# Kernel tuning notes

Measured on AMD Instinct MI355X. Metric: run time of the kernel, lower is better.

The kernel has to match this reference:

```python
import jax, jax.numpy as jnp
import numpy as np

B = 8
INPUT_SIZE = 32        # fc output dim == res row length
RESAMPLING = 500       # chunk width; 500->250->125->62->31 under 4 stride-2 pools
CHUNKS = 15            # == channel_size; seq length T = CHUNKS * RESAMPLING
T = CHUNKS * RESAMPLING
EPS = 1e-5
FC_IN = 32 * 6 * 31    # 5952 = flattened (C,H,W) embedding output


def _conv2d(x, w, b, pad):
    y = jax.lax.conv_general_dilated(x, w, (1, 1), pad,
                                     dimension_numbers=('NCHW', 'OIHW', 'NCHW'))
    return y + b[None, :, None, None]


def _bn(x, g, beta, m, v):
    # eval-mode BatchNorm2d with running stats
    scale = g / jnp.sqrt(v + EPS)
    return (x - m[None, :, None, None]) * scale[None, :, None, None] + beta[None, :, None, None]


def _maxpool22(x):
    return jax.lax.reduce_window(x, -jnp.inf, jax.lax.max, (1, 1, 2, 2), (1, 1, 2, 2), 'VALID')


def _forward(x, w1, b1, g1, beta1, m1, v1, w2, b2, g2, beta2, m2, v2,
             w3, b3, g3, beta3, m3, v3, w4, b4, g4, beta4, m4, v4,
             wfc, bfc, wc3, bc3, wout, bout):
    bsz = x.shape[0]
    # Vectorize the original per-sample / per-chunk Python loops:
    # split each [100, T] sample into CHUNKS windows of width RESAMPLING.
    h = x[:, 0].reshape(bsz, 100, CHUNKS, RESAMPLING)
    h = h.transpose(0, 2, 1, 3).reshape(bsz * CHUNKS, 1, 100, RESAMPLING)
    for w, b, g, bt, m, v in ((w1, b1, g1, beta1, m1, v1),
                              (w2, b2, g2, beta2, m2, v2),
                              (w3, b3, g3, beta3, m3, v3),
                              (w4, b4, g4, beta4, m4, v4)):
        h = _maxpool22(jax.nn.relu(_bn(_conv2d(h, w, b, [(2, 2), (2, 2)]), g, bt, m, v)))
    feats = h.reshape(bsz * CHUNKS, FC_IN)          # torch flattens in (C,H,W) order
    res = feats @ wfc.T + bfc                       # [B*15, 32]
    r = res.reshape(bsz, CHUNKS, INPUT_SIZE)[..., None]  # [B, 15, 32, 1] (NCHW)

    pad_c = lambda t: jnp.pad(t, ((0, 0), (0, 0), (1, 1), (0, 0)))   # ZeroPad2d((0,0,1,1))
    conv3 = lambda t: _conv2d(t, wc3, bc3, [(0, 0), (0, 0)])          # (3,1) conv
    r = conv3(jax.nn.relu(pad_c(r)))
    r = conv3(jax.nn.relu(pad_c(r)))
    while r.shape[2] > 2:  # static shapes: H 32->16->8->4->2
        p = jnp.pad(r, ((0, 0), (0, 0), (0, 1), (0, 0)))              # ZeroPad2d((0,0,0,1))
        px = jax.lax.reduce_window(p, -jnp.inf, jax.lax.max, (1, 1, 3, 1), (1, 1, 2, 2), 'VALID')
        t = conv3(jax.nn.relu(pad_c(px)))
        t = conv3(jax.nn.relu(pad_c(t)))
        r = t + px
    return r.reshape(bsz, 2 * CHUNKS) @ wout.T + bout  # [B, 2]


def setup_inputs() -> dict:
    key = jax.random.key(0)
    ks = jax.random.split(key, 16)

    def rn(k, shape, s):
        return jax.random.normal(k, shape, jnp.float32) * s

    inp = {"x": jax.random.normal(ks[0], (B, 1, 100, T), jnp.float32)}
    chans = [(1, 16), (16, 32), (32, 64), (64, 32)]
    for i, (ci, co) in enumerate(chans, 1):
        inp[f"w{i}"] = rn(ks[i], (co, ci, 5, 5), (2.0 / (ci * 25)) ** 0.5)
        inp[f"b{i}"] = jnp.zeros((co,), jnp.float32)
        inp[f"g{i}"] = jnp.ones((co,), jnp.float32)
        inp[f"beta{i}"] = jnp.zeros((co,), jnp.float32)
        inp[f"m{i}"] = jnp.zeros((co,), jnp.float32)
        inp[f"v{i}"] = jnp.ones((co,), jnp.float32)
    inp["wfc"] = rn(ks[5], (INPUT_SIZE, FC_IN), FC_IN ** -0.5)
    inp["bfc"] = jnp.zeros((INPUT_SIZE,), jnp.float32)
    inp["wc3"] = rn(ks[6], (CHUNKS, CHUNKS, 3, 1), (CHUNKS * 3) ** -0.5)
    inp["bc3"] = jnp.zeros((CHUNKS,), jnp.float32)
    inp["wout"] = rn(ks[7], (2, 2 * CHUNKS), (2 * CHUNKS) ** -0.5)
    inp["bout"] = jnp.zeros((2,), jnp.float32)
    return inp


def reference(x, w1, b1, g1, beta1, m1, v1, w2, b2, g2, beta2, m2, v2,
              w3, b3, g3, beta3, m3, v3, w4, b4, g4, beta4, m4, v4,
              wfc, bfc, wc3, bc3, wout, bout):
    return _forward(x, w1, b1, g1, beta1, m1, v1, w2, b2, g2, beta2, m2, v2,
                    w3, b3, g3, beta3, m3, v3, w4, b4, g4, beta4, m4, v4,
                    wfc, bfc, wc3, bc3, wout, bout)
```

## Files before the change

### kernel.cpp

```cpp
#include <hip/hip_runtime.h>
#include <hip/hip_bf16.h>

#define EPS 1e-5f

typedef short bf16x8 __attribute__((ext_vector_type(8)));
typedef float f32x4  __attribute__((ext_vector_type(4)));

__device__ __forceinline__ unsigned short f2bf(float f) {
    __hip_bfloat16 h = __float2bfloat16(f);
    return *(unsigned short*)&h;
}
__device__ __forceinline__ float bf2f(unsigned short u) {
    __hip_bfloat16 h = *(__hip_bfloat16*)&u;
    return __bfloat162float(h);
}

__global__ void prep_scsh(
    const float* g2, const float* be2, const float* m2, const float* v2, const float* b2,
    const float* g3, const float* be3, const float* m3, const float* v3, const float* b3,
    const float* g4, const float* be4, const float* m4, const float* v4, const float* b4,
    float* base)
{
    const int t = threadIdx.x;
    if (t < 32) {
        const float sc = g2[t] / sqrtf(v2[t] + EPS);
        base[t] = sc; base[32 + t] = (b2[t] - m2[t]) * sc + be2[t];
    } else if (t < 96) {
        const int c = t - 32;
        const float sc = g3[c] / sqrtf(v3[c] + EPS);
        base[64 + c] = sc; base[128 + c] = (b3[c] - m3[c]) * sc + be3[c];
    } else if (t < 128) {
        const int c = t - 96;
        const float sc = g4[c] / sqrtf(v4[c] + EPS);
        base[192 + c] = sc; base[224 + c] = (b4[c] - m4[c]) * sc + be4[c];
    }
}

template <int CI, int CO, int NP>
__global__ void prep_A(const float* __restrict__ w, unsigned short* __restrict__ Apk)
{
    constexpr int COTALL = CO / 16;
    const int tot = NP * COTALL * 512;
    for (int i = blockIdx.x * 256 + threadIdx.x; i < tot; i += gridDim.x * 256) {
        const int j = i & 7, lane = (i >> 3) & 63, pc = i >> 9;
        const int p = pc / COTALL, cot = pc % COTALL;
        const int kidx = p * 32 + (lane >> 4) * 8 + j;
        const int tap = kidx / CI, ci = kidx % CI;
        const int co = cot * 16 + (lane & 15);
        const float val = (tap < 25) ? w[((size_t)co * CI + ci) * 25 + tap] : 0.f;
        Apk[i] = f2bf(val);
    }
}

__global__ void prep_fcw(const float* __restrict__ wfc, unsigned short* __restrict__ wfcT)
{
    for (int i = blockIdx.x * 256 + threadIdx.x; i < 32 * 5952; i += gridDim.x * 256) {
        const int o = i / 5952, j = i % 5952;
        const int c = j & 31, yx = j >> 5;
        wfcT[i] = f2bf(wfc[(size_t)o * 5952 + c * 186 + yx]);
    }
}

__global__ __launch_bounds__(256) void conv1_kernel(
    const float* __restrict__ x,
    const float* __restrict__ w, const float* __restrict__ bias,
    const float* __restrict__ g, const float* __restrict__ beta,
    const float* __restrict__ m, const float* __restrict__ v,
    unsigned short* __restrict__ out)
{
    __shared__ float wlds[16 * 25];
    __shared__ float scb[16], shb[16];
    const int n = blockIdx.z;
    for (int i = threadIdx.x; i < 16 * 25; i += 256) wlds[i] = w[i];
    if (threadIdx.x < 16) {
        const int co = threadIdx.x;
        const float sc = g[co] / sqrtf(v[co] + EPS);
        scb[co] = sc;
        shb[co] = (bias[co] - m[co]) * sc + beta[co];
    }
    __syncthreads();

    const int sp = blockIdx.x * 256 + threadIdx.x;
    if (sp >= 50 * 250) return;
    const int ph = sp / 250, pw = sp % 250;
    const int b = n / 15, c = n % 15;
    const float* xb = x + (size_t)b * 100 * 7500 + (size_t)c * 500;

    const int y0 = 2 * ph - 2, x0 = 2 * pw - 2;
    float win[6][6];
    #pragma unroll
    for (int r = 0; r < 6; ++r) {
        const int y = y0 + r;
        const bool yv = (y >= 0 && y < 100);
        const float* row = xb + y * 7500;
        #pragma unroll
        for (int cc = 0; cc < 6; ++cc) {
            const int xx = x0 + cc;
            win[r][cc] = (yv && xx >= 0 && xx < 500) ? row[xx] : 0.f;
        }
    }

    unsigned int packed[8];
    #pragma unroll
    for (int oc = 0; oc < 16; ++oc) {
        const float* wc = &wlds[oc * 25];
        float a00 = 0.f, a01 = 0.f, a10 = 0.f, a11 = 0.f;
        #pragma unroll
        for (int kh = 0; kh < 5; ++kh)
            #pragma unroll
            for (int kw = 0; kw < 5; ++kw) {
                const float wv = wc[kh * 5 + kw];
                a00 += win[kh][kw] * wv;     a01 += win[kh][kw + 1] * wv;
                a10 += win[kh + 1][kw] * wv; a11 += win[kh + 1][kw + 1] * wv;
            }
        const float sc = scb[oc], sh = shb[oc];
        a00 = fmaxf(a00 * sc + sh, 0.f); a01 = fmaxf(a01 * sc + sh, 0.f);
        a10 = fmaxf(a10 * sc + sh, 0.f); a11 = fmaxf(a11 * sc + sh, 0.f);
        const unsigned short bits = f2bf(fmaxf(fmaxf(a00, a01), fmaxf(a10, a11)));
        if (oc & 1) packed[oc >> 1] |= ((unsigned int)bits) << 16;
        else        packed[oc >> 1] = bits;
    }
    unsigned short* dst = out + (((size_t)n * 50 + ph) * 250 + pw) * 16;
    *(uint4*)(dst)     = make_uint4(packed[0], packed[1], packed[2], packed[3]);
    *(uint4*)(dst + 8) = make_uint4(packed[4], packed[5], packed[6], packed[7]);
}

template <int CI, int CO, int H, int W, int PH, int PW, int NP>
__global__ __launch_bounds__(256) void mfma_conv(
    const unsigned short* __restrict__ in,
    const unsigned short* __restrict__ Apk,
    const float* __restrict__ sc, const float* __restrict__ sh,
    unsigned short* __restrict__ outp)
{
    constexpr int TH = 8, TW = 32, ROWS = TH + 4, COLS = TW + 4;
    constexpr int CSTR = CI * 2 + 16;
    constexpr int COTALL = CO / 16, COB = CO / 32;
    constexpr int CPC = CI / 8;
    __shared__ char smem[ROWS * COLS * CSTR];

    const int n = blockIdx.z / COB, cob = blockIdx.z % COB;
    const int ytile = blockIdx.y * TH, xtile = blockIdx.x * TW;
    const int tid = threadIdx.x;

    for (int i = tid; i < ROWS * COLS * CPC; i += 256) {
        const int cell = i / CPC, ch = i % CPC;
        const int yy = cell / COLS, xx = cell % COLS;
        const int gy = ytile - 2 + yy, gx = xtile - 2 + xx;
        uint4 val = make_uint4(0, 0, 0, 0);
        if (gy >= 0 && gy < H && gx >= 0 && gx < W)
            val = *(const uint4*)(in + ((((size_t)n * H + gy) * W + gx) * CI + ch * 8));
        *(uint4*)(smem + (size_t)(yy * COLS + xx) * CSTR + ch * 16) = val;
    }
    __syncthreads();

    const int lane = tid & 63, wav = tid >> 6;
    const int g = lane >> 4, c15 = lane & 15;
    const int laneCi = (CI == 16) ? ((g & 1) * 16) : (g * 16);
    const bool hi = (lane >= 32);

    int baddr[2][2];
    #pragma unroll
    for (int r = 0; r < 2; ++r)
        #pragma unroll
        for (int cg = 0; cg < 2; ++cg)
            baddr[r][cg] = ((wav * 2 + r) * COLS + cg * 16 + c15) * CSTR + laneCi;

    f32x4 acc[2][2][2] = {};

    #pragma unroll
    for (int p = 0; p < NP; ++p) {
        int D;
        if (CI == 16) {
            int t0 = p * 2;     if (t0 > 24) t0 = 24;
            int t1 = p * 2 + 1; if (t1 > 24) t1 = 24;
            const int D0 = ((t0 / 5) * COLS + t0 % 5) * CSTR;
            const int D1 = ((t1 / 5) * COLS + t1 % 5) * CSTR;
            D = hi ? D1 : D0;
        } else {
            const int tap = (CI == 32) ? p : (p >> 1);
            D = ((tap / 5) * COLS + tap % 5) * CSTR + ((CI == 64) ? (p & 1) * 64 : 0);
        }
        bf16x8 a[2], b[2][2];
        #pragma unroll
        for (int ct = 0; ct < 2; ++ct)
            a[ct] = *(const bf16x8*)(Apk + ((size_t)(p * COTALL + cob * 2 + ct) * 64 + lane) * 8);
        #pragma unroll
        for (int r = 0; r < 2; ++r)
            #pragma unroll
            for (int cg = 0; cg < 2; ++cg)
                b[r][cg] = *(const bf16x8*)(smem + baddr[r][cg] + D);
        #pragma unroll
        for (int r = 0; r < 2; ++r)
            #pragma unroll
            for (int ct = 0; ct < 2; ++ct)
                #pragma unroll
                for (int cg = 0; cg < 2; ++cg)
                    acc[r][ct][cg] = __builtin_amdgcn_mfma_f32_16x16x32_bf16(
                        a[ct], b[r][cg], acc[r][ct][cg], 0, 0, 0);
    }

    const int py = blockIdx.y * 4 + wav;
    #pragma unroll
    for (int ct = 0; ct < 2; ++ct) {
        const int coW = cob * 32 + ct * 16;
        const float4 scv = *(const float4*)(sc + coW + g * 4);
        const float4 shv = *(const float4*)(sh + coW + g * 4);
        #pragma unroll
        for (int cg = 0; cg < 2; ++cg) {
            const int px = (xtile >> 1) + cg * 8 + (c15 >> 1);
            ushort4 st;
            #pragma unroll
            for (int reg = 0; reg < 4; ++reg) {
                const float scr = (&scv.x)[reg], shr = (&shv.x)[reg];
                const float v0 = fmaxf(acc[0][ct][cg][reg] * scr + shr, 0.f);
                const float v1 = fmaxf(acc[1][ct][cg][reg] * scr + shr, 0.f);
                float mx = fmaxf(v0, v1);
                mx = fmaxf(mx, __shfl_xor(mx, 1));
                (&st.x)[reg] = f2bf(mx);
            }
            if ((lane & 1) == 0 && py < PH && px < PW)
                *(ushort4*)(outp + (((size_t)n * PH + py) * PW + px) * CO + coW + g * 4) = st;
        }
    }
}

__global__ __launch_bounds__(256) void fc_kernel(
    const unsigned short* __restrict__ feats, const unsigned short* __restrict__ wfcT,
    const float* __restrict__ bfc, float* __restrict__ res)
{
    const int n = blockIdx.x;
    const int lane = threadIdx.x & 63;
    const int wave = threadIdx.x >> 6;
    const unsigned short* f = feats + (size_t)n * 5952;
    #pragma unroll
    for (int o8 = 0; o8 < 8; ++o8) {
        const int o = wave * 8 + o8;
        const unsigned short* wr = wfcT + (size_t)o * 5952;
        float s = 0.f;
        #pragma unroll
        for (int i = 0; i < 12; ++i) {
            const int j8 = (i * 64 + lane) * 8;
            if (j8 < 5952) {
                const bf16x8 fv = *(const bf16x8*)(f + j8);
                const bf16x8 wv = *(const bf16x8*)(wr + j8);
                #pragma unroll
                for (int q = 0; q < 8; ++q)
                    s += bf2f(((const unsigned short*)&fv)[q]) *
                         bf2f(((const unsigned short*)&wv)[q]);
            }
        }
        #pragma unroll
        for (int off = 32; off > 0; off >>= 1) s += __shfl_down(s, off, 64);
        if (lane == 0) res[n * 32 + o] = s + bfc[o];
    }
}

__global__ __launch_bounds__(512) void dpcnn_kernel(
    const float* __restrict__ res,
    const float* __restrict__ wc3, const float* __restrict__ bc3,
    const float* __restrict__ wout, const float* __restrict__ bout,
    float* __restrict__ out)
{
    __shared__ float rr[8][15][32];
    __shared__ float ar[8][15][34];
    __shared__ float tr[8][15][34];
    __shared__ float px[8][15][16];
    __shared__ float wk[15][45];
    __shared__ float bk[15];

    const int tid = threadIdx.x;
    for (int i = tid; i < 15 * 45; i += 512) ((float*)wk)[i] = wc3[i];
    if (tid < 15) bk[tid] = bc3[tid];
    for (int i = tid; i < 8 * 15 * 32; i += 512) {
        const int h = i & 31, c = (i >> 5) % 15, b = i / 480;
        const float val = res[i];
        rr[b][c][h] = val;
        ar[b][c][h + 1] = fmaxf(val, 0.f);
    }
    for (int i = tid; i < 8 * 15; i += 512) {
        const int c = i % 15, b = i / 15;
        ar[b][c][0] = 0.f; ar[b][c][33] = 0.f;
        tr[b][c][0] = 0.f; tr[b][c][33] = 0.f;
    }
    __syncthreads();

    #define CONV45(SRC, BCH, CCH, HH)                                          \
        float s0 = bk[CCH], s1 = 0.f, s2 = 0.f;                                \
        {                                                                      \
            const float* srow = &SRC[BCH][0][HH];                              \
            const float* wrow = &wk[CCH][0];                                   \
            _Pragma("unroll")                                                  \
            for (int ci = 0; ci < 15; ++ci) {                                  \
                s0 += wrow[ci * 3 + 0] * srow[ci * 34 + 0];                    \
                s1 += wrow[ci * 3 + 1] * srow[ci * 34 + 1];                    \
                s2 += wrow[ci * 3 + 2] * srow[ci * 34 + 2];                    \
            }                                                                  \
        }                                                                      \
        const float val = s0 + s1 + s2;

    {
        for (int i = tid; i < 8 * 15 * 32; i += 512) {
            const int h = i & 31, cc = (i >> 5) % 15, b = i / 480;
            CONV45(ar, b, cc, h)
            tr[b][cc][h + 1] = fmaxf(val, 0.f);
        }
        __syncthreads();
        for (int i = tid; i < 8 * 15 * 32; i += 512) {
            const int h = i & 31, cc = (i >> 5) % 15, b = i / 480;
            CONV45(tr, b, cc, h)
            rr[b][cc][h] = val;
            ar[b][cc][h + 1] = fmaxf(val, 0.f);
        }
        __syncthreads();
    }

    for (int H = 32; H > 2; H >>= 1) {
        const int Hh = H >> 1;
        const int NE = 8 * 15 * Hh;
        for (int i = tid; i < NE; i += 512) {
            const int h = i % Hh, cc = (i / Hh) % 15, b = i / (15 * Hh);
            const float m0 = rr[b][cc][2 * h], m1 = rr[b][cc][2 * h + 1];
            const float m2 = (2 * h + 2 < H) ? rr[b][cc][2 * h + 2] : 0.f;
            const float pv = fmaxf(fmaxf(m0, m1), m2);
            px[b][cc][h] = pv;
            ar[b][cc][h + 1] = fmaxf(pv, 0.f);
            if (h == 0) ar[b][cc][0] = 0.f;
            if (h == Hh - 1) ar[b][cc][Hh + 1] = 0.f;
        }
        __syncthreads();
        for (int i = tid; i < NE; i += 512) {
            const int h = i % Hh, cc = (i / Hh) % 15, b = i / (15 * Hh);
            CONV45(ar, b, cc, h)
            tr[b][cc][h + 1] = fmaxf(val, 0.f);
            if (h == 0) tr[b][cc][0] = 0.f;
            if (h == Hh - 1) tr[b][cc][Hh + 1] = 0.f;
        }
        __syncthreads();
        for (int i = tid; i < NE; i += 512) {
            const int h = i % Hh, cc = (i / Hh) % 15, b = i / (15 * Hh);
            CONV45(tr, b, cc, h)
            const float rv = val + px[b][cc][h];
            rr[b][cc][h] = rv;
            ar[b][cc][h + 1] = fmaxf(rv, 0.f);
        }
        __syncthreads();
    }
    #undef CONV45

    if (tid < 16) {
        const int b = tid >> 1, o = tid & 1;
        float s = bout[o];
        for (int c = 0; c < 15; ++c)
            #pragma unroll
            for (int h = 0; h < 2; ++h)
                s += wout[o * 30 + c * 2 + h] * rr[b][c][h];
        out[b * 2 + o] = s;
    }
}

extern "C" void kernel_launch(void* const* d_in, const int* in_sizes, int n_in,
                              void* d_out, int out_size, void* d_ws, size_t ws_size,
                              hipStream_t stream)
{
    const float* x = (const float*)d_in[0];
    const float* w1 = (const float*)d_in[1];  const float* b1 = (const float*)d_in[2];
    const float* g1 = (const float*)d_in[3];  const float* be1 = (const float*)d_in[4];
    const float* m1 = (const float*)d_in[5];  const float* v1 = (const float*)d_in[6];
    const float* w2 = (const float*)d_in[7];  const float* b2 = (const float*)d_in[8];
    const float* g2 = (const float*)d_in[9];  const float* be2 = (const float*)d_in[10];
    const float* m2 = (const float*)d_in[11]; const float* v2 = (const float*)d_in[12];
    const float* w3 = (const float*)d_in[13]; const float* b3 = (const float*)d_in[14];
    const float* g3 = (const float*)d_in[15]; const float* be3 = (const float*)d_in[16];
    const float* m3 = (const float*)d_in[17]; const float* v3 = (const float*)d_in[18];
    const float* w4 = (const float*)d_in[19]; const float* b4 = (const float*)d_in[20];
    const float* g4 = (const float*)d_in[21]; const float* be4 = (const float*)d_in[22];
    const float* m4 = (const float*)d_in[23]; const float* v4 = (const float*)d_in[24];
    const float* wfc = (const float*)d_in[25]; const float* bfc = (const float*)d_in[26];
    const float* wc3 = (const float*)d_in[27]; const float* bc3 = (const float*)d_in[28];
    const float* wout = (const float*)d_in[29]; const float* bout = (const float*)d_in[30];
    float* out = (float*)d_out;

    (void)in_sizes; (void)n_in; (void)out_size; (void)ws_size;

    float* wsf = (float*)d_ws;
    float* res   = wsf;
    float* scsh  = wsf + 3840;
    float* sc2 = scsh, *sh2 = scsh + 32;
    float* sc3 = scsh + 64, *sh3 = scsh + 128;
    float* sc4 = scsh + 192, *sh4 = scsh + 224;
    unsigned short* A2  = (unsigned short*)(wsf + 4096);
    unsigned short* A3  = (unsigned short*)(wsf + 10752);
    unsigned short* A4  = (unsigned short*)(wsf + 36352);
    unsigned short* c1o = (unsigned short*)(wsf + 61952);
    unsigned short* c2o = (unsigned short*)(wsf + 12061952);
    unsigned short* c3o = (unsigned short*)(wsf + 18061952);
    unsigned short* c4o = (unsigned short*)(wsf + 20918912);
    unsigned short* wfcT = (unsigned short*)(wsf + 21276032);

    prep_scsh<<<1, 256, 0, stream>>>(g2, be2, m2, v2, b2,
                                     g3, be3, m3, v3, b3,
                                     g4, be4, m4, v4, b4, scsh);
    prep_A<16, 32, 13><<<52, 256, 0, stream>>>(w2, A2);
    prep_A<32, 64, 25><<<200, 256, 0, stream>>>(w3, A3);
    prep_A<64, 32, 50><<<200, 256, 0, stream>>>(w4, A4);
    prep_fcw<<<744, 256, 0, stream>>>(wfc, wfcT);

    conv1_kernel<<<dim3(49, 1, 120), 256, 0, stream>>>(
        x, w1, b1, g1, be1, m1, v1, c1o);
    mfma_conv<16, 32, 50, 250, 25, 125, 13><<<dim3(8, 7, 120), 256, 0, stream>>>(
        c1o, A2, sc2, sh2, c2o);
    mfma_conv<32, 64, 25, 125, 12, 62, 25><<<dim3(4, 3, 240), 256, 0, stream>>>(
        c2o, A3, sc3, sh3, c3o);
    mfma_conv<64, 32, 12, 62, 6, 31, 50><<<dim3(2, 2, 120), 256, 0, stream>>>(
        c3o, A4, sc4, sh4, c4o);
    fc_kernel<<<dim3(120), 256, 0, stream>>>(c4o, wfcT, bfc, res);
    dpcnn_kernel<<<dim3(1), 512, 0, stream>>>(res, wc3, bc3, wout, bout, out);
}
```

Before: 377.4 us.

## Run first conv layer on MFMA with bf16 input tile in LDS

Replaces the scalar FP32 conv1 kernel, which computes a 6x6 window and 16 output channels per thread, with a kernel that stages a bf16 input tile in shared memory and uses 16x16x32 bf16 MFMA with pre-packed weights. The 25 taps are padded to 32 with masking, and the BN scale and shift are precomputed in the prep kernel. The 2x2 max-pool is done with a row pair per wave plus a lane shuffle. This moves conv1 from VALU FMAs to matrix cores. It quantizes the raw input to bf16, which costs accuracy, and workspace offsets were shifted to make room for the new buffers.

```diff
diff --git a/kernel.cpp b/kernel.cpp
--- a/kernel.cpp
+++ b/kernel.cpp
@@ -16,6 +16,7 @@
 }
 
 __global__ void prep_scsh(
+    const float* g1, const float* be1, const float* m1, const float* v1, const float* b1,
     const float* g2, const float* be2, const float* m2, const float* v2, const float* b2,
     const float* g3, const float* be3, const float* m3, const float* v3, const float* b3,
     const float* g4, const float* be4, const float* m4, const float* v4, const float* b4,
@@ -33,6 +34,10 @@
         const int c = t - 96;
         const float sc = g4[c] / sqrtf(v4[c] + EPS);
         base[192 + c] = sc; base[224 + c] = (b4[c] - m4[c]) * sc + be4[c];
+    } else if (t < 144) {
+        const int c = t - 128;
+        const float sc = g1[c] / sqrtf(v1[c] + EPS);
+        base[256 + c] = sc; base[272 + c] = (b1[c] - m1[c]) * sc + be1[c];
     }
 }
 
@@ -52,6 +57,17 @@
     }
 }
 
+__global__ void prep_A1(const float* __restrict__ w, unsigned short* __restrict__ Apk)
+{
+    const int i = threadIdx.x;
+    if (i < 512) {
+        const int j = i & 7, lane = i >> 3;
+        const int k = ((lane >> 4) & 3) * 8 + j;
+        const int co = lane & 15;
+        Apk[i] = f2bf((k < 25) ? w[co * 25 + k] : 0.f);
+    }
+}
+
 __global__ void prep_fcw(const float* __restrict__ wfc, unsigned short* __restrict__ wfcT)
 {
     for (int i = blockIdx.x * 256 + threadIdx.x; i < 32 * 5952; i += gridDim.x * 256) {
@@ -61,68 +77,76 @@
     }
 }
 
-__global__ __launch_bounds__(256) void conv1_kernel(
+__global__ __launch_bounds__(256) void conv1_mfma(
     const float* __restrict__ x,
-    const float* __restrict__ w, const float* __restrict__ bias,
-    const float* __restrict__ g, const float* __restrict__ beta,
-    const float* __restrict__ m, const float* __restrict__ v,
+    const unsigned short* __restrict__ Apk1,
+    const float* __restrict__ sc, const float* __restrict__ sh,
     unsigned short* __restrict__ out)
 {
-    __shared__ float wlds[16 * 25];
-    __shared__ float scb[16], shb[16];
+    constexpr int RSTR = 38;
+    __shared__ unsigned short tile[12 * RSTR];
     const int n = blockIdx.z;
-    for (int i = threadIdx.x; i < 16 * 25; i += 256) wlds[i] = w[i];
-    if (threadIdx.x < 16) {
-        const int co = threadIdx.x;
-        const float sc = g[co] / sqrtf(v[co] + EPS);
-        scb[co] = sc;
-        shb[co] = (bias[co] - m[co]) * sc + beta[co];
-    }
-    __syncthreads();
-
-    const int sp = blockIdx.x * 256 + threadIdx.x;
-    if (sp >= 50 * 250) return;
-    const int ph = sp / 250, pw = sp % 250;
+    const int y0 = blockIdx.y * 8, x0 = blockIdx.x * 32;
     const int b = n / 15, c = n % 15;
     const float* xb = x + (size_t)b * 100 * 7500 + (size_t)c * 500;
-
-    const int y0 = 2 * ph - 2, x0 = 2 * pw - 2;
-    float win[6][6];
-    #pragma unroll
-    for (int r = 0; r < 6; ++r) {
-        const int y = y0 + r;
-        const bool yv = (y >= 0 && y < 100);
-        const float* row = xb + y * 7500;
-        #pragma unroll
-        for (int cc = 0; cc < 6; ++cc) {
-            const int xx = x0 + cc;
-            win[r][cc] = (yv && xx >= 0 && xx < 500) ? row[xx] : 0.f;
-        }
-    }
-
-    unsigned int packed[8];
-    #pragma unroll
-    for (int oc = 0; oc < 16; ++oc) {
-        const float* wc = &wlds[oc * 25];
-        float a00 = 0.f, a01 = 0.f, a10 = 0.f, a11 = 0.f;
-        #pragma unroll
-        for (int kh = 0; kh < 5; ++kh)
+    const int tid = threadIdx.x;
+
+    for (int i = tid; i < 12 * 36; i += 256) {
+        const int yy = i / 36, xx = i % 36;
+        const int gy = y0 - 2 + yy, gx = x0 - 2 + xx;
+        float v = 0.f;
+        if (gy >= 0 && gy < 100 && gx >= 0 && gx < 500) v = xb[gy * 7500 + gx];
+        tile[yy * RSTR + xx] = f2bf(v);
+    }
+
+    const int lane = tid & 63, wav = tid >> 6;
+    const int g = lane >> 4, c15 = lane & 15;
+    const bf16x8 a = *(const bf16x8*)(Apk1 + lane * 8);
+
+    int off[8]; unsigned short msk[8];
+    #pragma unroll
+    for (int j = 0; j < 8; ++j) {
+        int tap = g * 8 + j;
+        msk[j] = (tap < 25) ? 0xFFFFu : 0u;
+        if (tap > 24) tap = 24;
+        off[j] = (tap / 5) * RSTR + (tap % 5);
+    }
+    __syncthreads();
+
+    f32x4 acc[2][2] = {};
+    #pragma unroll
+    for (int r = 0; r < 2; ++r)
+        #pragma unroll
+        for (int cg = 0; cg < 2; ++cg) {
+            const int base = (2 * wav + r) * RSTR + cg * 16 + c15;
+            bf16x8 bfrag;
             #pragma unroll
-            for (int kw = 0; kw < 5; ++kw) {
-                const float wv = wc[kh * 5 + kw];
-                a00 += win[kh][kw] * wv;     a01 += win[kh][kw + 1] * wv;
-                a10 += win[kh + 1][kw] * wv; a11 += win[kh + 1][kw + 1] * wv;
+            for (int j = 0; j < 8; ++j) {
+                const unsigned short v = tile[base + off[j]] & msk[j];
+                ((unsigned short*)&bfrag)[j] = (short)v;
             }
-        const float sc = scb[oc], sh = shb[oc];
-        a00 = fmaxf(a00 * sc + sh, 0.f); a01 = fmaxf(a01 * sc + sh, 0.f);
-        a10 = fmaxf(a10 * sc + sh, 0.f); a11 = fmaxf(a11 * sc + sh, 0.f);
-        const unsigned short bits = f2bf(fmaxf(fmaxf(a00, a01), fmaxf(a10, a11)));
-        if (oc & 1) packed[oc >> 1] |= ((unsigned int)bits) << 16;
-        else        packed[oc >> 1] = bits;
-    }
-    unsigned short* dst = out + (((size_t)n * 50 + ph) * 250 + pw) * 16;
-    *(uint4*)(dst)     = make_uint4(packed[0], packed[1], packed[2], packed[3]);
-    *(uint4*)(dst + 8) = make_uint4(packed[4], packed[5], packed[6], packed[7]);
+            acc[r][cg] = __builtin_amdgcn_mfma_f32_16x16x32_bf16(a, bfrag, acc[r][cg], 0, 0, 0);
+        }
+
+    const int py = blockIdx.y * 4 + wav;
+    const float4 scv = *(const float4*)(sc + g * 4);
+    const float4 shv = *(const float4*)(sh + g * 4);
+    #pragma unroll
+    for (int cg = 0; cg < 2; ++cg) {
+        const int px = (x0 >> 1) + cg * 8 + (c15 >> 1);
+        ushort4 st;
+        #pragma unroll
+        for (int reg = 0; reg < 4; ++reg) {
+            const float scr = (&scv.x)[reg], shr = (&shv.x)[reg];
+            const float v0 = fmaxf(acc[0][cg][reg] * scr + shr, 0.f);
+            const float v1 = fmaxf(acc[1][cg][reg] * scr + shr, 0.f);
+            float mx = fmaxf(v0, v1);
+            mx = fmaxf(mx, __shfl_xor(mx, 1));
+            (&st.x)[reg] = f2bf(mx);
+        }
+        if ((lane & 1) == 0 && py < 50 && px < 250)
+            *(ushort4*)(out + (((size_t)n * 50 + py) * 250 + px) * 16 + g * 4) = st;
+    }
 }
 
 template <int CI, int CO, int H, int W, int PH, int PW, int NP>
@@ -388,25 +412,28 @@
     float* sc2 = scsh, *sh2 = scsh + 32;
     float* sc3 = scsh + 64, *sh3 = scsh + 128;
     float* sc4 = scsh + 192, *sh4 = scsh + 224;
-    unsigned short* A2  = (unsigned short*)(wsf + 4096);
-    unsigned short* A3  = (unsigned short*)(wsf + 10752);
-    unsigned short* A4  = (unsigned short*)(wsf + 36352);
-    unsigned short* c1o = (unsigned short*)(wsf + 61952);
-    unsigned short* c2o = (unsigned short*)(wsf + 12061952);
-    unsigned short* c3o = (unsigned short*)(wsf + 18061952);
-    unsigned short* c4o = (unsigned short*)(wsf + 20918912);
-    unsigned short* wfcT = (unsigned short*)(wsf + 21276032);
-
-    prep_scsh<<<1, 256, 0, stream>>>(g2, be2, m2, v2, b2,
+    float* sc1 = scsh + 256, *sh1 = scsh + 272;
+    unsigned short* A1  = (unsigned short*)(wsf + 4160);
+    unsigned short* A2  = (unsigned short*)(wsf + 4416);
+    unsigned short* A3  = (unsigned short*)(wsf + 11072);
+    unsigned short* A4  = (unsigned short*)(wsf + 36672);
+    unsigned short* c1o = (unsigned short*)(wsf + 62272);
+    unsigned short* c2o = (unsigned short*)(wsf + 12062272);
+    unsigned short* c3o = (unsigned short*)(wsf + 18062272);
+    unsigned short* c4o = (unsigned short*)(wsf + 20919232);
+    unsigned short* wfcT = (unsigned short*)(wsf + 21276352);
+
+    prep_scsh<<<1, 256, 0, stream>>>(g1, be1, m1, v1, b1,
+                                     g2, be2, m2, v2, b2,
                                      g3, be3, m3, v3, b3,
                                      g4, be4, m4, v4, b4, scsh);
+    prep_A1<<<1, 512, 0, stream>>>(w1, A1);
     prep_A<16, 32, 13><<<52, 256, 0, stream>>>(w2, A2);
     prep_A<32, 64, 25><<<200, 256, 0, stream>>>(w3, A3);
     prep_A<64, 32, 50><<<200, 256, 0, stream>>>(w4, A4);
     prep_fcw<<<744, 256, 0, stream>>>(wfc, wfcT);
 
-    conv1_kernel<<<dim3(49, 1, 120), 256, 0, stream>>>(
-        x, w1, b1, g1, be1, m1, v1, c1o);
+    conv1_mfma<<<dim3(16, 13, 120), 256, 0, stream>>>(x, A1, sc1, sh1, c1o);
     mfma_conv<16, 32, 50, 250, 25, 125, 13><<<dim3(8, 7, 120), 256, 0, stream>>>(
         c1o, A2, sc2, sh2, c2o);
     mfma_conv<32, 64, 25, 125, 12, 62, 25><<<dim3(4, 3, 240), 256, 0, stream>>>(
```

Result: faster. 352.1 us (-6.7%).
